# Kernel tuning notes

Measured on AMD Instinct MI355X. Metric: run time of the kernel, lower is better.

## Reference

```python
import jax, jax.numpy as jnp
import numpy as np

B, T, H = 16, 512, 768
S = 32            # gold spans per example
L = 50            # max_span_len -> candidate ends per span
NT = 3            # num_types
HS = 4 * H        # span repr size


def setup_inputs() -> dict:
    key = jax.random.key(0)
    ks = jax.random.split(key, 8)
    h = jax.random.normal(ks[0], (B, T, H), dtype=jnp.float32)
    attention_mask = jnp.ones((B, T), dtype=jnp.int32)
    starts = jax.random.randint(ks[1], (B, S), 1, 400).astype(jnp.int32)
    lens = jax.random.randint(ks[2], (B, S), 0, L).astype(jnp.int32)
    ends = starts + lens                      # <= 448 < last_tok=510
    types = jax.random.randint(ks[3], (B, S), 0, NT).astype(jnp.int32)
    W1 = jax.random.normal(ks[4], (HS, HS), dtype=jnp.float32) * (1.0 / np.sqrt(HS))
    b1 = jnp.zeros((HS,), dtype=jnp.float32)
    w_score = jax.random.normal(ks[5], (HS,), dtype=jnp.float32) * (1.0 / np.sqrt(HS))
    b_score = jnp.zeros((1,), dtype=jnp.float32)
    W_type = jax.random.normal(ks[6], (HS, NT), dtype=jnp.float32) * (1.0 / np.sqrt(HS))
    b_type = jnp.zeros((NT,), dtype=jnp.float32)
    return {"h": h, "attention_mask": attention_mask, "span_starts": starts,
            "span_ends": ends, "span_types": types, "W1": W1, "b1": b1,
            "w_score": w_score, "b_score": b_score, "W_type": W_type, "b_type": b_type}


def _span_loss(h, attention_mask, span_starts, span_ends, span_types,
               W1, b1, w_score, b_score, W_type, b_type, type_loss_weight=1.0):
    cls = h[:, 0]                                              # [B,H]
    # prefix sums for O(1) segment means: pre[b,t] = sum h[b,0:t]
    pre = jnp.concatenate([jnp.zeros((B, 1, H), h.dtype), jnp.cumsum(h, axis=1)], axis=1)

    valid_len = attention_mask.sum(axis=1)                     # [B]
    last_tok = jnp.maximum(1, valid_len - 2)                   # [B]

    s = span_starts                                            # [B,S]
    e_gold = span_ends
    gold_idx = e_gold - s                                      # [B,S]
    lt = last_tok[:, None]
    span_valid = (s >= 1) & (s <= lt) & (e_gold >= s) & (e_gold <= lt) & (gold_idx < L)

    e_max = jnp.minimum(s + L - 1, lt)                         # [B,S]
    p = s[..., None] + jnp.arange(L, dtype=s.dtype)            # [B,S,L] candidate ends
    cand_valid = p <= e_max[..., None]

    sc = jnp.clip(s, 0, T - 1)
    pc = jnp.clip(p, 0, T - 1)
    bi2 = jnp.arange(B)[:, None]
    bi3 = jnp.arange(B)[:, None, None]

    h_start = h[bi2, sc]                                       # [B,S,H]
    h_end = h[bi3, pc]                                         # [B,S,L,H]
    seg_len = jnp.maximum(p - s[..., None] + 1, 1).astype(h.dtype)
    h_mean = (pre[bi3, pc + 1] - pre[bi2, sc][:, :, None]) / seg_len[..., None]

    repr_ = jnp.concatenate([
        jnp.broadcast_to(h_start[:, :, None], (B, S, L, H)),
        h_end,
        h_mean,
        jnp.broadcast_to(cls[:, None, None], (B, S, L, H)),
    ], axis=-1)                                                # [B,S,L,4H]

    h1 = jax.nn.gelu(jnp.einsum('bslh,hd->bsld', repr_, W1) + b1, approximate=False)
    scores = jnp.einsum('bsld,d->bsl', h1, w_score) + b_score[0]      # [B,S,L]
    type_logits = jnp.einsum('bsld,dk->bslk', h1, W_type) + b_type    # [B,S,L,NT]

    # end-index CE over valid candidate ends
    masked = jnp.where(cand_valid, scores, jnp.float32(-1e9))
    logp_end = jax.nn.log_softmax(masked, axis=-1)             # [B,S,L]
    gi = jnp.clip(gold_idx, 0, L - 1)
    end_loss = -jnp.take_along_axis(logp_end, gi[..., None], axis=-1)[..., 0]  # [B,S]

    # type CE at the gold end index
    tl_gold = jnp.take_along_axis(type_logits, gi[..., None, None], axis=2)[:, :, 0]  # [B,S,NT]
    logp_t = jax.nn.log_softmax(tl_gold, axis=-1)
    tg = jnp.clip(span_types, 0, NT - 1)
    type_loss = -jnp.take_along_axis(logp_t, tg[..., None], axis=-1)[..., 0]  # [B,S]

    vmask = span_valid.astype(h.dtype)
    n_seg = vmask.sum()
    denom = jnp.maximum(n_seg, 1.0)
    loss_end = jnp.where(n_seg > 0, (end_loss * vmask).sum() / denom, 0.0)
    loss_type = jnp.where(n_seg > 0, (type_loss * vmask).sum() / denom, 0.0)
    return loss_end + type_loss_weight * loss_type


def reference(h, attention_mask, span_starts, span_ends, span_types,
              W1, b1, w_score, b_score, W_type, b_type):
    return _span_loss(h, attention_mask, span_starts, span_ends, span_types,
                      W1, b1, w_score, b_score, W_type, b_type)
```

## Files before the change

kernel.cpp:

```cpp
#include <hip/hip_runtime.h>
#include <hip/hip_bf16.h>
#include <math.h>

#define B_ 16
#define T_ 512
#define H_ 768
#define S_ 32
#define L_ 50
#define NT_ 3
#define HS_ 3072
#define CH_ 32
#define CT_ 16

#define TX_ 464
#define YB2 7424
#define GB 14848
#define CLSB 15360
#define XYROWS 14848
#define AROWS 15616
#define NKT 24
#define SLOT_SH 16384

typedef __attribute__((ext_vector_type(8))) short short8;
typedef __attribute__((ext_vector_type(4))) float f32x4;

__device__ __forceinline__ unsigned short f2bf(float f) {
    __hip_bfloat16 b = __float2bfloat16(f);
    return *(unsigned short*)&b;
}
__device__ __forceinline__ float bf2f(unsigned short u) {
    union { unsigned int i; float f; } v; v.i = ((unsigned int)u) << 16; return v.f;
}
__device__ __forceinline__ void load_lds16(const void* g, void* l) {
    __builtin_amdgcn_global_load_lds((__attribute__((address_space(1))) void*)g,
                                     (__attribute__((address_space(3))) void*)l, 16, 0, 0);
}
__device__ __forceinline__ ushort4 pack4(float4 v) {
    ushort4 o; o.x = f2bf(v.x); o.y = f2bf(v.y); o.z = f2bf(v.z); o.w = f2bf(v.w);
    return o;
}

__device__ __forceinline__ float gelu_exact(float v) {
    float a = fabsf(v) * 0.70710678118654752f;
    float t = __builtin_amdgcn_rcpf(fmaf(a, 0.47047f, 1.0f));
    float poly = t * fmaf(t, fmaf(t, 0.7478556f, -0.0958798f), 0.3480242f);
    float e = __builtin_amdgcn_exp2f(a * a * -1.4426950408889634f);
    float erfa = fmaf(-poly, e, 1.0f);
    float erfv = copysignf(erfa, v);
    return 0.5f * v * (1.0f + erfv);
}

__global__ __launch_bounds__(256) void cumsum_pass1(const float4* __restrict__ h4,
                                                    float4* __restrict__ partial) {
    int idx = blockIdx.x * 256 + threadIdx.x;
    int hd4 = idx % 192; int t = idx / 192; int ch = t % CH_; int b = t / CH_;
    const float4* hp = h4 + ((size_t)b * T_ + ch * CT_) * 192 + hd4;
    float4 acc = {0.f, 0.f, 0.f, 0.f};
#pragma unroll
    for (int tt = 0; tt < CT_; tt++) {
        float4 v = hp[(size_t)tt * 192];
        acc.x += v.x; acc.y += v.y; acc.z += v.z; acc.w += v.w;
    }
    partial[idx] = acc;
}

__global__ __launch_bounds__(256) void cumsum_pass3(const float4* __restrict__ h4,
                                                    const float4* __restrict__ partial,
                                                    ushort4* __restrict__ Ab4) {
    int idx = blockIdx.x * 256 + threadIdx.x;
    int hd4 = idx % 192; int t = idx / 192; int ch = t % CH_; int b = t / CH_;
    if (ch * CT_ >= TX_) return;
    float4 acc = {0.f, 0.f, 0.f, 0.f};
#pragma unroll
    for (int c = 0; c < CH_; c++) {
        if (c < ch) {
            float4 v = partial[((size_t)b * CH_ + c) * 192 + hd4];
            acc.x += v.x; acc.y += v.y; acc.z += v.z; acc.w += v.w;
        }
    }
    const float4* hp = h4 + ((size_t)b * T_ + ch * CT_) * 192 + hd4;
    if (ch == 0) {
        ushort4 z = {0, 0, 0, 0};
        Ab4[((size_t)(YB2 + b * TX_)) * 192 + hd4] = z;
    }
#pragma unroll
    for (int tt = 0; tt < CT_; tt++) {
        int t2 = ch * CT_ + tt;
        float4 hv = hp[(size_t)tt * 192];
        if (t2 < TX_)
            Ab4[((size_t)(b * TX_ + t2)) * 192 + hd4] = pack4(hv);
        acc.x += hv.x; acc.y += hv.y; acc.z += hv.z; acc.w += hv.w;
        if (t2 + 1 < TX_)
            Ab4[((size_t)(YB2 + b * TX_ + t2 + 1)) * 192 + hd4] = pack4(acc);
    }
}

__global__ void gather_kernel(const float* __restrict__ h,
                              const int* __restrict__ starts,
                              __hip_bfloat16* __restrict__ Ab) {
    int r = blockIdx.x;
    int src_row, dst_row;
    if (r < B_ * S_) {
        int b = r / S_;
        int sv = starts[r];
        int sc = min(max(sv, 0), T_ - 1);
        src_row = b * T_ + sc;
        dst_row = GB + r;
    } else {
        int b = r - B_ * S_;
        src_row = b * T_;
        dst_row = CLSB + b;
    }
    __hip_bfloat16* dst = Ab + (size_t)dst_row * H_;
    const float* src = h + (size_t)src_row * H_;
    for (int j = threadIdx.x; j < H_; j += 256)
        dst[j] = __float2bfloat16(src[j]);
}

__global__ __launch_bounds__(256) void transpose_w(const float* __restrict__ W1,
                                                   __hip_bfloat16* __restrict__ Wt) {
    __shared__ float tile[64][65];
    int n0 = blockIdx.x * 64, k0 = blockIdx.y * 64;
    int c = threadIdx.x & 63, r0 = threadIdx.x >> 6;
#pragma unroll
    for (int i = 0; i < 16; i++) {
        int r = r0 + i * 4;
        tile[r][c] = W1[(size_t)(k0 + r) * HS_ + n0 + c];
    }
    __syncthreads();
    int p = k0 / H_, kl = k0 % H_;
    __hip_bfloat16* out = Wt + (size_t)p * HS_ * H_;
#pragma unroll
    for (int i = 0; i < 16; i++) {
        int r = r0 + i * 4;
        out[(size_t)(n0 + r) * H_ + kl + c] = __float2bfloat16(tile[c][r]);
    }
}

__device__ __forceinline__ void mfma16(const short8 (&a)[4], const short8 (&b)[4],
                                       f32x4 (&acc)[8][4], int off) {
#pragma unroll
    for (int mf = 0; mf < 4; ++mf)
#pragma unroll
        for (int nf = 0; nf < 4; ++nf)
            acc[off + mf][nf] = __builtin_amdgcn_mfma_f32_16x16x32_bf16(
                a[mf], b[nf], acc[off + mf][nf], 0, 0, 0);
}

#define STAGE_A(nslot, k0_) {                                                  \
    char* d_ = (char*)(nslot) + dstoff;                                        \
    load_lds16(pA + (k0_), d_);                                                \
    load_lds16(pA + (size_t)128 * H_ + (k0_), d_ + 8192);                      \
}
#define STAGE_B(nslot, k0_) {                                                  \
    char* d_ = (char*)(nslot) + 16384 + dstoff;                                \
    load_lds16(pB + (k0_), d_);                                                \
    load_lds16(pB + (size_t)128 * H_ + (k0_), d_ + 8192);                      \
}

#define TILE_STEP(kt, WAITSTR, DO_STAGE)                                       \
  {                                                                            \
    const short* slot = lds + ((kt) & 3) * SLOT_SH;                            \
    short* nslot = lds + (((kt) + 3) & 3) * SLOT_SH;                           \
    asm volatile(WAITSTR ::: "memory");                                        \
    __builtin_amdgcn_s_barrier();                                              \
    __builtin_amdgcn_sched_barrier(0);                                         \
    short8 a[4], b[4];                                                         \
    _Pragma("unroll")                                                          \
    for (int i = 0; i < 4; ++i)                                                \
      a[i] = *(const short8*)&slot[(wr * 128 + i * 16 + l15) * 32 + pcs];      \
    _Pragma("unroll")                                                          \
    for (int i = 0; i < 4; ++i)                                                \
      b[i] = *(const short8*)&slot[8192 + (wc * 64 + i * 16 + l15) * 32 + pcs];\
    if (DO_STAGE) { STAGE_A(nslot, ((kt) + 3) * 32) }                          \
    asm volatile("s_waitcnt lgkmcnt(0)" ::: "memory");                         \
    __builtin_amdgcn_sched_barrier(0);                                         \
    __builtin_amdgcn_s_setprio(1);                                             \
    mfma16(a, b, acc, 0);                                                      \
    __builtin_amdgcn_s_setprio(0);                                             \
    __builtin_amdgcn_s_barrier();                                              \
    __builtin_amdgcn_sched_barrier(0);                                         \
    _Pragma("unroll")                                                          \
    for (int i = 0; i < 4; ++i)                                                \
      a[i] = *(const short8*)&slot[(wr * 128 + 64 + i * 16 + l15) * 32 + pcs]; \
    if (DO_STAGE) { STAGE_B(nslot, ((kt) + 3) * 32) }                          \
    asm volatile("s_waitcnt lgkmcnt(0)" ::: "memory");                         \
    __builtin_amdgcn_sched_barrier(0);                                         \
    __builtin_amdgcn_s_setprio(1);                                             \
    mfma16(a, b, acc, 4);                                                      \
    __builtin_amdgcn_s_setprio(0);                                             \
  }

__global__ __launch_bounds__(512, 2) void mfma_gemm(const __hip_bfloat16* __restrict__ Ab,
                                                    const __hip_bfloat16* __restrict__ Wt,
                                                    __hip_bfloat16* __restrict__ XY,
                                                    float* __restrict__ ST,
                                                    float* __restrict__ CC) {
    __shared__ short lds[4 * SLOT_SH];
    int tid = threadIdx.x;
    int wave = tid >> 6, lane = tid & 63;
    int wr = wave >> 2, wc = wave & 3;
    int l15 = lane & 15;
    int pcs = ((lane >> 4) ^ ((l15 >> 1) & 3)) * 8;

    int orig = blockIdx.x;
    int xcd = orig & 7, loc = orig >> 3;
    int wg = (xcd < 4 ? xcd * 92 : 368 + (xcd - 4) * 91) + loc;
    int mt = wg / 12, nt = wg - mt * 12;
    int m0 = mt << 8, n0 = nt << 8;

    const __hip_bfloat16* Bt;
    if (m0 < YB2)        Bt = Wt + (size_t)1 * HS_ * H_;
    else if (m0 < GB)    Bt = Wt + (size_t)2 * HS_ * H_;
    else if (m0 < CLSB)  Bt = Wt;
    else                 Bt = Wt + (size_t)3 * HS_ * H_;

    int srow = wave * 16 + (lane >> 2);
    int lcS = ((lane & 3) ^ ((lane >> 3) & 3)) * 8;
    const __hip_bfloat16* pA = Ab + (size_t)(m0 + srow) * H_ + lcS;
    const __hip_bfloat16* pB = Bt + (size_t)(n0 + srow) * H_ + lcS;
    int dstoff = wave * 1024;

    f32x4 acc[8][4] = {};

#pragma unroll
    for (int t = 0; t < 3; ++t) {
        STAGE_A(lds + t * SLOT_SH, t * 32)
        STAGE_B(lds + t * SLOT_SH, t * 32)
    }

    for (int kt = 0; kt < NKT - 3; ++kt)
        TILE_STEP(kt, "s_waitcnt vmcnt(8)", true)
    TILE_STEP(NKT - 3, "s_waitcnt vmcnt(8)", false)
    TILE_STEP(NKT - 2, "s_waitcnt vmcnt(4)", false)
    TILE_STEP(NKT - 1, "s_waitcnt vmcnt(0)", false)

    int mb = m0 + wr * 128, nb = n0 + wc * 64;
#pragma unroll
    for (int mf = 0; mf < 8; ++mf) {
#pragma unroll
        for (int nf = 0; nf < 4; ++nf) {
            int n = nb + nf * 16 + l15;
            int mr = mb + mf * 16 + (lane >> 4) * 4;
#pragma unroll
            for (int r = 0; r < 4; ++r) {
                int m = mr + r;
                float v = acc[mf][nf][r];
                if (m < XYROWS) {
                    XY[(size_t)m * HS_ + n] = __float2bfloat16(v);
                } else if (m < CLSB) {
                    ST[(size_t)(m - GB) * HS_ + n] = v;
                } else if (m < CLSB + 16) {
                    CC[(size_t)(m - CLSB) * HS_ + n] = v;
                }
            }
        }
    }
}

__global__ __launch_bounds__(256) void c0_kernel(const float4* __restrict__ ST,
                                                 const float4* __restrict__ CC,
                                                 const float4* __restrict__ b1,
                                                 const float4* __restrict__ w_score,
                                                 ushort4* __restrict__ c0b,
                                                 ushort4* __restrict__ wb16) {
    if (blockIdx.x >= 512 * HS_ / 4 / 256) {
        int i = (blockIdx.x - 512 * HS_ / 4 / 256) * 256 + threadIdx.x;
        wb16[i] = pack4(w_score[i]);
        return;
    }
    int i = blockIdx.x * 256 + threadIdx.x;
    int row = i / (HS_ / 4);
    int b = row >> 5;
    int c4 = i % (HS_ / 4);
    float4 s = ST[i], c = CC[b * (HS_ / 4) + c4], bb = b1[c4];
    float4 v = {s.x + c.x + bb.x, s.y + c.y + bb.y, s.z + c.z + bb.z, s.w + c.w + bb.w};
    c0b[i] = pack4(v);
}

__global__ __launch_bounds__(256) void combine_kernel(
    const unsigned short* __restrict__ c0, const unsigned short* __restrict__ wb16,
    const __hip_bfloat16* __restrict__ XY,
    const float* __restrict__ b_score, const float* __restrict__ W_type,
    const int* __restrict__ starts, const int* __restrict__ ends,
    float* __restrict__ scores, float* __restrict__ tgold) {
    int x = blockIdx.x;
    int b = x & 15, s = x >> 4;
    int bs = b * S_ + s;
    int wave = threadIdx.x >> 6, lane = threadIdx.x & 63;
    int pr = blockIdx.y * 4 + wave;
    if (pr >= L_ / 2) return;
    int l0 = pr * 2, l1 = l0 + 1;
    int sv = starts[bs], ev = ends[bs];
    int gi = min(max(ev - sv, 0), L_ - 1);
    int sc = min(max(sv, 0), TX_ - 1);
    int pc0 = min(max(sv + l0, 0), TX_ - 2);
    int pc1 = min(max(sv + l1, 0), TX_ - 2);
    float inv0 = 1.0f / (float)(l0 + 1);
    float inv1 = 1.0f / (float)(l1 + 1);
    bool isg0 = (l0 == gi), isg1 = (l1 == gi);
    bool anyg = isg0 || isg1;

    const unsigned short* X0 = (const unsigned short*)(XY + (size_t)(b * TX_ + pc0) * HS_);
    const unsigned short* X1 = (const unsigned short*)(XY + (size_t)(b * TX_ + pc1) * HS_);
    const unsigned short* Y0 = (const unsigned short*)(XY + (size_t)(YB2 + b * TX_ + pc0 + 1) * HS_);
    const unsigned short* Y1 = (const unsigned short*)(XY + (size_t)(YB2 + b * TX_ + pc1 + 1) * HS_);
    const unsigned short* Ysr = (const unsigned short*)(XY + (size_t)(YB2 + b * TX_ + sc) * HS_);
    const unsigned short* c0r = c0 + (size_t)bs * HS_;

    float local0 = 0.f, local1 = 0.f, t0 = 0.f, t1 = 0.f, t2 = 0.f;
#pragma unroll
    for (int j = 0; j < 6; j++) {
        int d = j * 512 + lane * 8;
        short8 xv0 = *(const short8*)(X0 + d);
        short8 xv1 = *(const short8*)(X1 + d);
        short8 yv0 = *(const short8*)(Y0 + d);
        short8 yv1 = *(const short8*)(Y1 + d);
        short8 sv8 = *(const short8*)(Ysr + d);
        short8 cv8 = *(const short8*)(c0r + d);
        short8 wv8 = *(const short8*)(wb16 + d);
#pragma unroll
        for (int q = 0; q < 8; q++) {
            float ys = bf2f(((const unsigned short*)&sv8)[q]);
            float cv = bf2f(((const unsigned short*)&cv8)[q]);
            float w  = bf2f(((const unsigned short*)&wv8)[q]);
            float v0 = fmaf(bf2f(((const unsigned short*)&yv0)[q]) - ys, inv0, cv) +
                       bf2f(((const unsigned short*)&xv0)[q]);
            float v1 = fmaf(bf2f(((const unsigned short*)&yv1)[q]) - ys, inv1, cv) +
                       bf2f(((const unsigned short*)&xv1)[q]);
            float g0 = gelu_exact(v0);
            float g1 = gelu_exact(v1);
            local0 = fmaf(g0, w, local0);
            local1 = fmaf(g1, w, local1);
            if (anyg) {
                float gg = isg0 ? g0 : g1;
                t0 = fmaf(gg, W_type[(d + q) * NT_ + 0], t0);
                t1 = fmaf(gg, W_type[(d + q) * NT_ + 1], t1);
                t2 = fmaf(gg, W_type[(d + q) * NT_ + 2], t2);
            }
        }
    }
#pragma unroll
    for (int off = 32; off >= 1; off >>= 1) {
        local0 += __shfl_down(local0, off);
        local1 += __shfl_down(local1, off);
    }
    if (lane == 0) {
        float bs0 = b_score[0];
        scores[(size_t)bs * L_ + l0] = local0 + bs0;
        scores[(size_t)bs * L_ + l1] = local1 + bs0;
    }
    if (anyg) {
#pragma unroll
        for (int off = 32; off >= 1; off >>= 1) {
            t0 += __shfl_down(t0, off);
            t1 += __shfl_down(t1, off);
            t2 += __shfl_down(t2, off);
        }
        if (lane == 0) {
            tgold[bs * NT_ + 0] = t0;
            tgold[bs * NT_ + 1] = t1;
            tgold[bs * NT_ + 2] = t2;
        }
    }
}

__global__ __launch_bounds__(512) void loss_kernel(
    const float* __restrict__ scores, const float* __restrict__ tgold,
    const int* __restrict__ mask, const int* __restrict__ starts,
    const int* __restrict__ ends, const int* __restrict__ types,
    const float* __restrict__ b_type, float* __restrict__ out) {
    __shared__ int svl[B_];
    __shared__ float r[3][8];
    int tid = threadIdx.x;
    int b = tid / S_;
    if (tid < B_) svl[tid] = 0;
    __syncthreads();
    {
        int part = 0;
        const int* mp = mask + tid * 16;
#pragma unroll
        for (int i = 0; i < 16; i++) part += mp[i];
        atomicAdd(&svl[tid / (T_ / 16)], part);
    }
    __syncthreads();
    int vl = svl[b];
    int lt = max(1, vl - 2);
    int sv = starts[tid], ev = ends[tid];
    int gold = ev - sv;
    bool valid = (sv >= 1) && (sv <= lt) && (ev >= sv) && (ev <= lt) && (gold < L_);
    int emax = min(sv + L_ - 1, lt);
    const float* sp = scores + (size_t)tid * L_;
    float m = -1e30f;
    for (int l = 0; l < L_; l++) {
        float v = (sv + l <= emax) ? sp[l] : -1e9f;
        m = fmaxf(m, v);
    }
    float sum = 0.f;
    for (int l = 0; l < L_; l++) {
        float v = (sv + l <= emax) ? sp[l] : -1e9f;
        sum += expf(v - m);
    }
    int gi = min(max(gold, 0), L_ - 1);
    float vg = (sv + gi <= emax) ? sp[gi] : -1e9f;
    float end_loss = (m + logf(sum)) - vg;

    float t0 = tgold[tid * 3 + 0] + b_type[0];
    float t1 = tgold[tid * 3 + 1] + b_type[1];
    float t2 = tgold[tid * 3 + 2] + b_type[2];
    float tm = fmaxf(t0, fmaxf(t1, t2));
    float tsum = expf(t0 - tm) + expf(t1 - tm) + expf(t2 - tm);
    int tg = min(max(types[tid], 0), NT_ - 1);
    float tv = (tg == 0) ? t0 : ((tg == 1) ? t1 : t2);
    float type_loss = (tm + logf(tsum)) - tv;

    float ve = valid ? end_loss : 0.f;
    float vt = valid ? type_loss : 0.f;
    float vc = valid ? 1.f : 0.f;
    for (int off = 32; off >= 1; off >>= 1) {
        ve += __shfl_down(ve, off);
        vt += __shfl_down(vt, off);
        vc += __shfl_down(vc, off);
    }
    if ((tid & 63) == 0) {
        int w = tid >> 6;
        r[0][w] = ve; r[1][w] = vt; r[2][w] = vc;
    }
    __syncthreads();
    if (tid == 0) {
        float se = 0, st = 0, n = 0;
        for (int w = 0; w < 8; w++) { se += r[0][w]; st += r[1][w]; n += r[2][w]; }
        float denom = fmaxf(n, 1.f);
        out[0] = (n > 0.f) ? (se / denom + st / denom) : 0.f;
    }
}

extern "C" void kernel_launch(void* const* d_in, const int* in_sizes, int n_in,
                              void* d_out, int out_size, void* d_ws, size_t ws_size,
                              hipStream_t stream) {
    const float* h       = (const float*)d_in[0];
    const int*   mask    = (const int*)d_in[1];
    const int*   starts  = (const int*)d_in[2];
    const int*   ends    = (const int*)d_in[3];
    const int*   types   = (const int*)d_in[4];
    const float* W1      = (const float*)d_in[5];
    const float* b1      = (const float*)d_in[6];
    const float* w_score = (const float*)d_in[7];
    const float* b_score = (const float*)d_in[8];
    const float* W_type  = (const float*)d_in[9];
    const float* b_type  = (const float*)d_in[10];
    float* out = (float*)d_out;

    char* ws = (char*)d_ws;
    size_t off = 0;
    __hip_bfloat16* Ab = (__hip_bfloat16*)(ws + off); off += (size_t)AROWS * H_ * 2;
    __hip_bfloat16* XY = (__hip_bfloat16*)(ws + off); off += (size_t)XYROWS * HS_ * 2;
    __hip_bfloat16* Wt = (__hip_bfloat16*)(ws + off); off += (size_t)4 * HS_ * H_ * 2;
    float* ST     = (float*)(ws + off);               off += (size_t)512 * HS_ * 4;
    float* CC     = (float*)(ws + off);               off += (size_t)16 * HS_ * 4;
    unsigned short* c0b = (unsigned short*)(ws + off); off += (size_t)512 * HS_ * 2;
    unsigned short* wb16 = (unsigned short*)(ws + off); off += (size_t)HS_ * 2;
    float* scores = (float*)(ws + off);               off += (size_t)B_ * S_ * L_ * 4;
    float* tgold  = (float*)(ws + off);               off += (size_t)B_ * S_ * NT_ * 4;
    float4* partial = (float4*)XY;

    hipLaunchKernelGGL(cumsum_pass1, dim3(B_ * CH_ * 192 / 256), dim3(256), 0, stream,
                       (const float4*)h, partial);
    hipLaunchKernelGGL(cumsum_pass3, dim3(B_ * CH_ * 192 / 256), dim3(256), 0, stream,
                       (const float4*)h, (const float4*)partial, (ushort4*)Ab);
    hipLaunchKernelGGL(gather_kernel, dim3(B_ * S_ + B_), dim3(256), 0, stream, h, starts, Ab);
    hipLaunchKernelGGL(transpose_w, dim3(48, 48), dim3(256), 0, stream, W1, Wt);
    hipLaunchKernelGGL(mfma_gemm, dim3((AROWS / 256) * 12), dim3(512), 0, stream,
                       Ab, Wt, XY, ST, CC);
    hipLaunchKernelGGL(c0_kernel, dim3(512 * HS_ / 4 / 256 + 3), dim3(256), 0, stream,
                       (const float4*)ST, (const float4*)CC, (const float4*)b1,
                       (const float4*)w_score, (ushort4*)c0b, (ushort4*)wb16);
    hipLaunchKernelGGL(combine_kernel, dim3(B_ * S_, 7), dim3(256), 0, stream,
                       c0b, wb16, XY, b_score, W_type, starts, ends, scores, tgold);
    hipLaunchKernelGGL(loss_kernel, dim3(1), dim3(512), 0, stream,
                       scores, tgold, mask, starts, ends, types, b_type, out);
}
```

Baseline: 317.2 us.

## Fuse gather into cumsum pass and c0 into combine, drop GEMM sched barrier

Merges the gather kernel into cumsum_pass3 as extra blocks, and removes the c0_kernel by computing ST+CC+b1 and the bf16 w_score inside combine_kernel, whose grid shrinks from 7 y-blocks to 1 with each wave looping over span-length pairs. It also drops one sched_barrier in the GEMM inner loop. The aim is fewer launches and no c0b/wb16 round trip through memory. In exchange, combine has less parallelism (512 blocks instead of about 3584), holds the per-span c0 vector in registers, and the GEMM instruction schedule may shift.

```diff
diff --git a/kernel.cpp b/kernel.cpp
--- a/kernel.cpp
+++ b/kernel.cpp
@@ -66,7 +66,29 @@
 
 __global__ __launch_bounds__(256) void cumsum_pass3(const float4* __restrict__ h4,
                                                     const float4* __restrict__ partial,
-                                                    ushort4* __restrict__ Ab4) {
+                                                    ushort4* __restrict__ Ab4,
+                                                    const float* __restrict__ h,
+                                                    const int* __restrict__ starts) {
+    if (blockIdx.x >= B_ * CH_ * 192 / 256) {
+        int r = blockIdx.x - B_ * CH_ * 192 / 256;
+        int src_row, dst_row;
+        if (r < B_ * S_) {
+            int b = r / S_;
+            int sv = starts[r];
+            int sc = min(max(sv, 0), T_ - 1);
+            src_row = b * T_ + sc;
+            dst_row = GB + r;
+        } else {
+            int b = r - B_ * S_;
+            src_row = b * T_;
+            dst_row = CLSB + b;
+        }
+        __hip_bfloat16* dst = (__hip_bfloat16*)Ab4 + (size_t)dst_row * H_;
+        const float* src = h + (size_t)src_row * H_;
+        for (int j = threadIdx.x; j < H_; j += 256)
+            dst[j] = __float2bfloat16(src[j]);
+        return;
+    }
     int idx = blockIdx.x * 256 + threadIdx.x;
     int hd4 = idx % 192; int t = idx / 192; int ch = t % CH_; int b = t / CH_;
     if (ch * CT_ >= TX_) return;
@@ -93,28 +115,6 @@
         if (t2 + 1 < TX_)
             Ab4[((size_t)(YB2 + b * TX_ + t2 + 1)) * 192 + hd4] = pack4(acc);
     }
-}
-
-__global__ void gather_kernel(const float* __restrict__ h,
-                              const int* __restrict__ starts,
-                              __hip_bfloat16* __restrict__ Ab) {
-    int r = blockIdx.x;
-    int src_row, dst_row;
-    if (r < B_ * S_) {
-        int b = r / S_;
-        int sv = starts[r];
-        int sc = min(max(sv, 0), T_ - 1);
-        src_row = b * T_ + sc;
-        dst_row = GB + r;
-    } else {
-        int b = r - B_ * S_;
-        src_row = b * T_;
-        dst_row = CLSB + b;
-    }
-    __hip_bfloat16* dst = Ab + (size_t)dst_row * H_;
-    const float* src = h + (size_t)src_row * H_;
-    for (int j = threadIdx.x; j < H_; j += 256)
-        dst[j] = __float2bfloat16(src[j]);
 }
 
 __global__ __launch_bounds__(256) void transpose_w(const float* __restrict__ W1,
@@ -179,7 +179,6 @@
     mfma16(a, b, acc, 0);                                                      \
     __builtin_amdgcn_s_setprio(0);                                             \
     __builtin_amdgcn_s_barrier();                                              \
-    __builtin_amdgcn_sched_barrier(0);                                         \
     _Pragma("unroll")                                                          \
     for (int i = 0; i < 4; ++i)                                                \
       a[i] = *(const short8*)&slot[(wr * 128 + 64 + i * 16 + l15) * 32 + pcs]; \
@@ -258,28 +257,9 @@
     }
 }
 
-__global__ __launch_bounds__(256) void c0_kernel(const float4* __restrict__ ST,
-                                                 const float4* __restrict__ CC,
-                                                 const float4* __restrict__ b1,
-                                                 const float4* __restrict__ w_score,
-                                                 ushort4* __restrict__ c0b,
-                                                 ushort4* __restrict__ wb16) {
-    if (blockIdx.x >= 512 * HS_ / 4 / 256) {
-        int i = (blockIdx.x - 512 * HS_ / 4 / 256) * 256 + threadIdx.x;
-        wb16[i] = pack4(w_score[i]);
-        return;
-    }
-    int i = blockIdx.x * 256 + threadIdx.x;
-    int row = i / (HS_ / 4);
-    int b = row >> 5;
-    int c4 = i % (HS_ / 4);
-    float4 s = ST[i], c = CC[b * (HS_ / 4) + c4], bb = b1[c4];
-    float4 v = {s.x + c.x + bb.x, s.y + c.y + bb.y, s.z + c.z + bb.z, s.w + c.w + bb.w};
-    c0b[i] = pack4(v);
-}
-
 __global__ __launch_bounds__(256) void combine_kernel(
-    const unsigned short* __restrict__ c0, const unsigned short* __restrict__ wb16,
+    const float* __restrict__ ST, const float* __restrict__ CC,
+    const float* __restrict__ b1, const float* __restrict__ w_score,
     const __hip_bfloat16* __restrict__ XY,
     const float* __restrict__ b_score, const float* __restrict__ W_type,
     const int* __restrict__ starts, const int* __restrict__ ends,
@@ -288,79 +268,100 @@
     int b = x & 15, s = x >> 4;
     int bs = b * S_ + s;
     int wave = threadIdx.x >> 6, lane = threadIdx.x & 63;
-    int pr = blockIdx.y * 4 + wave;
-    if (pr >= L_ / 2) return;
-    int l0 = pr * 2, l1 = l0 + 1;
     int sv = starts[bs], ev = ends[bs];
     int gi = min(max(ev - sv, 0), L_ - 1);
     int sc = min(max(sv, 0), TX_ - 1);
-    int pc0 = min(max(sv + l0, 0), TX_ - 2);
-    int pc1 = min(max(sv + l1, 0), TX_ - 2);
-    float inv0 = 1.0f / (float)(l0 + 1);
-    float inv1 = 1.0f / (float)(l1 + 1);
-    bool isg0 = (l0 == gi), isg1 = (l1 == gi);
-    bool anyg = isg0 || isg1;
-
-    const unsigned short* X0 = (const unsigned short*)(XY + (size_t)(b * TX_ + pc0) * HS_);
-    const unsigned short* X1 = (const unsigned short*)(XY + (size_t)(b * TX_ + pc1) * HS_);
-    const unsigned short* Y0 = (const unsigned short*)(XY + (size_t)(YB2 + b * TX_ + pc0 + 1) * HS_);
-    const unsigned short* Y1 = (const unsigned short*)(XY + (size_t)(YB2 + b * TX_ + pc1 + 1) * HS_);
+    float bs0 = b_score[0];
+
+    union U8 { short8 s; unsigned short u[8]; };
+    short8 ysv[6], cv[6], wv[6];
     const unsigned short* Ysr = (const unsigned short*)(XY + (size_t)(YB2 + b * TX_ + sc) * HS_);
-    const unsigned short* c0r = c0 + (size_t)bs * HS_;
-
-    float local0 = 0.f, local1 = 0.f, t0 = 0.f, t1 = 0.f, t2 = 0.f;
+    const float* STr = ST + (size_t)bs * HS_;
+    const float* CCr = CC + (size_t)b * HS_;
 #pragma unroll
     for (int j = 0; j < 6; j++) {
         int d = j * 512 + lane * 8;
-        short8 xv0 = *(const short8*)(X0 + d);
-        short8 xv1 = *(const short8*)(X1 + d);
-        short8 yv0 = *(const short8*)(Y0 + d);
-        short8 yv1 = *(const short8*)(Y1 + d);
-        short8 sv8 = *(const short8*)(Ysr + d);
-        short8 cv8 = *(const short8*)(c0r + d);
-        short8 wv8 = *(const short8*)(wb16 + d);
-#pragma unroll
-        for (int q = 0; q < 8; q++) {
-            float ys = bf2f(((const unsigned short*)&sv8)[q]);
-            float cv = bf2f(((const unsigned short*)&cv8)[q]);
-            float w  = bf2f(((const unsigned short*)&wv8)[q]);
-            float v0 = fmaf(bf2f(((const unsigned short*)&yv0)[q]) - ys, inv0, cv) +
-                       bf2f(((const unsigned short*)&xv0)[q]);
-            float v1 = fmaf(bf2f(((const unsigned short*)&yv1)[q]) - ys, inv1, cv) +
-                       bf2f(((const unsigned short*)&xv1)[q]);
-            float g0 = gelu_exact(v0);
-            float g1 = gelu_exact(v1);
-            local0 = fmaf(g0, w, local0);
-            local1 = fmaf(g1, w, local1);
-            if (anyg) {
-                float gg = isg0 ? g0 : g1;
-                t0 = fmaf(gg, W_type[(d + q) * NT_ + 0], t0);
-                t1 = fmaf(gg, W_type[(d + q) * NT_ + 1], t1);
-                t2 = fmaf(gg, W_type[(d + q) * NT_ + 2], t2);
+        ysv[j] = *(const short8*)(Ysr + d);
+        float4 sa = *(const float4*)(STr + d),     sb = *(const float4*)(STr + d + 4);
+        float4 ca = *(const float4*)(CCr + d),     cb = *(const float4*)(CCr + d + 4);
+        float4 ba = *(const float4*)(b1 + d),      bb = *(const float4*)(b1 + d + 4);
+        U8 uc;
+        uc.u[0] = f2bf(sa.x + ca.x + ba.x); uc.u[1] = f2bf(sa.y + ca.y + ba.y);
+        uc.u[2] = f2bf(sa.z + ca.z + ba.z); uc.u[3] = f2bf(sa.w + ca.w + ba.w);
+        uc.u[4] = f2bf(sb.x + cb.x + bb.x); uc.u[5] = f2bf(sb.y + cb.y + bb.y);
+        uc.u[6] = f2bf(sb.z + cb.z + bb.z); uc.u[7] = f2bf(sb.w + cb.w + bb.w);
+        cv[j] = uc.s;
+        float4 wa = *(const float4*)(w_score + d), wb = *(const float4*)(w_score + d + 4);
+        U8 uw;
+        uw.u[0] = f2bf(wa.x); uw.u[1] = f2bf(wa.y); uw.u[2] = f2bf(wa.z); uw.u[3] = f2bf(wa.w);
+        uw.u[4] = f2bf(wb.x); uw.u[5] = f2bf(wb.y); uw.u[6] = f2bf(wb.z); uw.u[7] = f2bf(wb.w);
+        wv[j] = uw.s;
+    }
+
+    for (int pr = wave; pr < L_ / 2; pr += 4) {
+        int l0 = pr * 2, l1 = l0 + 1;
+        int pc0 = min(max(sv + l0, 0), TX_ - 2);
+        int pc1 = min(max(sv + l1, 0), TX_ - 2);
+        float inv0 = 1.0f / (float)(l0 + 1);
+        float inv1 = 1.0f / (float)(l1 + 1);
+        bool isg0 = (l0 == gi), isg1 = (l1 == gi);
+        bool anyg = isg0 || isg1;
+
+        const unsigned short* X0 = (const unsigned short*)(XY + (size_t)(b * TX_ + pc0) * HS_);
+        const unsigned short* X1 = (const unsigned short*)(XY + (size_t)(b * TX_ + pc1) * HS_);
+        const unsigned short* Y0 = (const unsigned short*)(XY + (size_t)(YB2 + b * TX_ + pc0 + 1) * HS_);
+        const unsigned short* Y1 = (const unsigned short*)(XY + (size_t)(YB2 + b * TX_ + pc1 + 1) * HS_);
+
+        float local0 = 0.f, local1 = 0.f, t0 = 0.f, t1 = 0.f, t2 = 0.f;
+#pragma unroll
+        for (int j = 0; j < 6; j++) {
+            int d = j * 512 + lane * 8;
+            short8 xv0 = *(const short8*)(X0 + d);
+            short8 xv1 = *(const short8*)(X1 + d);
+            short8 yv0 = *(const short8*)(Y0 + d);
+            short8 yv1 = *(const short8*)(Y1 + d);
+#pragma unroll
+            for (int q = 0; q < 8; q++) {
+                float ys = bf2f(((const unsigned short*)&ysv[j])[q]);
+                float cvq = bf2f(((const unsigned short*)&cv[j])[q]);
+                float w  = bf2f(((const unsigned short*)&wv[j])[q]);
+                float v0 = fmaf(bf2f(((const unsigned short*)&yv0)[q]) - ys, inv0, cvq) +
+                           bf2f(((const unsigned short*)&xv0)[q]);
+                float v1 = fmaf(bf2f(((const unsigned short*)&yv1)[q]) - ys, inv1, cvq) +
+                           bf2f(((const unsigned short*)&xv1)[q]);
+                float g0 = gelu_exact(v0);
+                float g1 = gelu_exact(v1);
+                local0 = fmaf(g0, w, local0);
+                local1 = fmaf(g1, w, local1);
+                if (anyg) {
+                    float gg = isg0 ? g0 : g1;
+                    t0 = fmaf(gg, W_type[(d + q) * NT_ + 0], t0);
+                    t1 = fmaf(gg, W_type[(d + q) * NT_ + 1], t1);
+                    t2 = fmaf(gg, W_type[(d + q) * NT_ + 2], t2);
+                }
             }
         }
-    }
-#pragma unroll
-    for (int off = 32; off >= 1; off >>= 1) {
-        local0 += __shfl_down(local0, off);
-        local1 += __shfl_down(local1, off);
-    }
-    if (lane == 0) {
-        float bs0 = b_score[0];
-        scores[(size_t)bs * L_ + l0] = local0 + bs0;
-        scores[(size_t)bs * L_ + l1] = local1 + bs0;
-    }
-    if (anyg) {
 #pragma unroll
         for (int off = 32; off >= 1; off >>= 1) {
-            t0 += __shfl_down(t0, off);
-            t1 += __shfl_down(t1, off);
-            t2 += __shfl_down(t2, off);
+            local0 += __shfl_down(local0, off);
+            local1 += __shfl_down(local1, off);
         }
         if (lane == 0) {
-            tgold[bs * NT_ + 0] = t0;
-            tgold[bs * NT_ + 1] = t1;
-            tgold[bs * NT_ + 2] = t2;
+            scores[(size_t)bs * L_ + l0] = local0 + bs0;
+            scores[(size_t)bs * L_ + l1] = local1 + bs0;
+        }
+        if (anyg) {
+#pragma unroll
+            for (int off = 32; off >= 1; off >>= 1) {
+                t0 += __shfl_down(t0, off);
+                t1 += __shfl_down(t1, off);
+                t2 += __shfl_down(t2, off);
+            }
+            if (lane == 0) {
+                tgold[bs * NT_ + 0] = t0;
+                tgold[bs * NT_ + 1] = t1;
+                tgold[bs * NT_ + 2] = t2;
+            }
         }
     }
 }
@@ -458,25 +459,21 @@
     __hip_bfloat16* Wt = (__hip_bfloat16*)(ws + off); off += (size_t)4 * HS_ * H_ * 2;
     float* ST     = (float*)(ws + off);               off += (size_t)512 * HS_ * 4;
     float* CC     = (float*)(ws + off);               off += (size_t)16 * HS_ * 4;
-    unsigned short* c0b = (unsigned short*)(ws + off); off += (size_t)512 * HS_ * 2;
-    unsigned short* wb16 = (unsigned short*)(ws + off); off += (size_t)HS_ * 2;
     float* scores = (float*)(ws + off);               off += (size_t)B_ * S_ * L_ * 4;
     float* tgold  = (float*)(ws + off);               off += (size_t)B_ * S_ * NT_ * 4;
     float4* partial = (float4*)XY;
 
     hipLaunchKernelGGL(cumsum_pass1, dim3(B_ * CH_ * 192 / 256), dim3(256), 0, stream,
                        (const float4*)h, partial);
-    hipLaunchKernelGGL(cumsum_pass3, dim3(B_ * CH_ * 192 / 256), dim3(256), 0, stream,
-                       (const float4*)h, (const float4*)partial, (ushort4*)Ab);
-    hipLaunchKernelGGL(gather_kernel, dim3(B_ * S_ + B_), dim3(256), 0, stream, h, starts, Ab);
+    hipLaunchKernelGGL(cumsum_pass3, dim3(B_ * CH_ * 192 / 256 + B_ * S_ + B_), dim3(256),
+                       0, stream, (const float4*)h, (const float4*)partial, (ushort4*)Ab,
+                       h, starts);
     hipLaunchKernelGGL(transpose_w, dim3(48, 48), dim3(256), 0, stream, W1, Wt);
     hipLaunchKernelGGL(mfma_gemm, dim3((AROWS / 256) * 12), dim3(512), 0, stream,
                        Ab, Wt, XY, ST, CC);
-    hipLaunchKernelGGL(c0_kernel, dim3(512 * HS_ / 4 / 256 + 3), dim3(256), 0, stream,
-                       (const float4*)ST, (const float4*)CC, (const float4*)b1,
-                       (const float4*)w_score, (ushort4*)c0b, (ushort4*)wb16);
-    hipLaunchKernelGGL(combine_kernel, dim3(B_ * S_, 7), dim3(256), 0, stream,
-                       c0b, wb16, XY, b_score, W_type, starts, ends, scores, tgold);
+    hipLaunchKernelGGL(combine_kernel, dim3(B_ * S_), dim3(256), 0, stream,
+                       ST, CC, b1, w_score, XY, b_score, W_type, starts, ends,
+                       scores, tgold);
     hipLaunchKernelGGL(loss_kernel, dim3(1), dim3(512), 0, stream,
                        scores, tgold, mask, starts, ends, types, b_type, out);
 }
```

Measured after the change: 371.8 us. +17.2%, slower.

## Restructure combine kernel around token windows staged in LDS; fuse gather into cumsum

Applied to the files above, without the earlier changes.

The combine kernel is reorganized so each block owns a window of 5 token positions for one batch row. It stages the X/Y rows for those positions and the score weights into LDS, then iterates over all spans whose candidate ends fall in the window. Each X/Y row is read from global memory once per window rather than once per (span, candidate) pair, which cuts redundant HBM/L2 traffic. The gather kernel is folded into cumsum_pass3 as extra blocks, saving a launch, and one sched_barrier is dropped in the GEMM macro. The trade-offs are a serial loop over all 32 spans per block, uneven work per window, and higher LDS use (about 66KB) that limits occupancy.

```diff
diff --git a/kernel.cpp b/kernel.cpp
--- a/kernel.cpp
+++ b/kernel.cpp
@@ -20,6 +20,8 @@
 #define AROWS 15616
 #define NKT 24
 #define SLOT_SH 16384
+#define WW 5
+#define NWIN 90
 
 typedef __attribute__((ext_vector_type(8))) short short8;
 typedef __attribute__((ext_vector_type(4))) float f32x4;
@@ -66,7 +68,29 @@
 
 __global__ __launch_bounds__(256) void cumsum_pass3(const float4* __restrict__ h4,
                                                     const float4* __restrict__ partial,
-                                                    ushort4* __restrict__ Ab4) {
+                                                    ushort4* __restrict__ Ab4,
+                                                    const float* __restrict__ h,
+                                                    const int* __restrict__ starts) {
+    if (blockIdx.x >= B_ * CH_ * 192 / 256) {
+        int r = blockIdx.x - B_ * CH_ * 192 / 256;
+        int src_row, dst_row;
+        if (r < B_ * S_) {
+            int b = r / S_;
+            int sv = starts[r];
+            int sc = min(max(sv, 0), T_ - 1);
+            src_row = b * T_ + sc;
+            dst_row = GB + r;
+        } else {
+            int b = r - B_ * S_;
+            src_row = b * T_;
+            dst_row = CLSB + b;
+        }
+        __hip_bfloat16* dst = (__hip_bfloat16*)Ab4 + (size_t)dst_row * H_;
+        const float* src = h + (size_t)src_row * H_;
+        for (int j = threadIdx.x; j < H_; j += 256)
+            dst[j] = __float2bfloat16(src[j]);
+        return;
+    }
     int idx = blockIdx.x * 256 + threadIdx.x;
     int hd4 = idx % 192; int t = idx / 192; int ch = t % CH_; int b = t / CH_;
     if (ch * CT_ >= TX_) return;
@@ -93,28 +117,6 @@
         if (t2 + 1 < TX_)
             Ab4[((size_t)(YB2 + b * TX_ + t2 + 1)) * 192 + hd4] = pack4(acc);
     }
-}
-
-__global__ void gather_kernel(const float* __restrict__ h,
-                              const int* __restrict__ starts,
-                              __hip_bfloat16* __restrict__ Ab) {
-    int r = blockIdx.x;
-    int src_row, dst_row;
-    if (r < B_ * S_) {
-        int b = r / S_;
-        int sv = starts[r];
-        int sc = min(max(sv, 0), T_ - 1);
-        src_row = b * T_ + sc;
-        dst_row = GB + r;
-    } else {
-        int b = r - B_ * S_;
-        src_row = b * T_;
-        dst_row = CLSB + b;
-    }
-    __hip_bfloat16* dst = Ab + (size_t)dst_row * H_;
-    const float* src = h + (size_t)src_row * H_;
-    for (int j = threadIdx.x; j < H_; j += 256)
-        dst[j] = __float2bfloat16(src[j]);
 }
 
 __global__ __launch_bounds__(256) void transpose_w(const float* __restrict__ W1,
@@ -179,7 +181,6 @@
     mfma16(a, b, acc, 0);                                                      \
     __builtin_amdgcn_s_setprio(0);                                             \
     __builtin_amdgcn_s_barrier();                                              \
-    __builtin_amdgcn_sched_barrier(0);                                         \
     _Pragma("unroll")                                                          \
     for (int i = 0; i < 4; ++i)                                                \
       a[i] = *(const short8*)&slot[(wr * 128 + 64 + i * 16 + l15) * 32 + pcs]; \
@@ -278,90 +279,101 @@
     c0b[i] = pack4(v);
 }
 
-__global__ __launch_bounds__(256) void combine_kernel(
-    const unsigned short* __restrict__ c0, const unsigned short* __restrict__ wb16,
+__global__ __launch_bounds__(512, 4) void combine_kernel(
+    const unsigned short* __restrict__ c0b, const unsigned short* __restrict__ wb16,
     const __hip_bfloat16* __restrict__ XY,
     const float* __restrict__ b_score, const float* __restrict__ W_type,
     const int* __restrict__ starts, const int* __restrict__ ends,
     float* __restrict__ scores, float* __restrict__ tgold) {
+    __shared__ unsigned short xL[WW * HS_];
+    __shared__ unsigned short yL[WW * HS_];
+    __shared__ unsigned short wL[HS_];
     int x = blockIdx.x;
-    int b = x & 15, s = x >> 4;
-    int bs = b * S_ + s;
-    int wave = threadIdx.x >> 6, lane = threadIdx.x & 63;
-    int pr = blockIdx.y * 4 + wave;
-    if (pr >= L_ / 2) return;
-    int l0 = pr * 2, l1 = l0 + 1;
-    int sv = starts[bs], ev = ends[bs];
-    int gi = min(max(ev - sv, 0), L_ - 1);
-    int sc = min(max(sv, 0), TX_ - 1);
-    int pc0 = min(max(sv + l0, 0), TX_ - 2);
-    int pc1 = min(max(sv + l1, 0), TX_ - 2);
-    float inv0 = 1.0f / (float)(l0 + 1);
-    float inv1 = 1.0f / (float)(l1 + 1);
-    bool isg0 = (l0 == gi), isg1 = (l1 == gi);
-    bool anyg = isg0 || isg1;
-
-    const unsigned short* X0 = (const unsigned short*)(XY + (size_t)(b * TX_ + pc0) * HS_);
-    const unsigned short* X1 = (const unsigned short*)(XY + (size_t)(b * TX_ + pc1) * HS_);
-    const unsigned short* Y0 = (const unsigned short*)(XY + (size_t)(YB2 + b * TX_ + pc0 + 1) * HS_);
-    const unsigned short* Y1 = (const unsigned short*)(XY + (size_t)(YB2 + b * TX_ + pc1 + 1) * HS_);
-    const unsigned short* Ysr = (const unsigned short*)(XY + (size_t)(YB2 + b * TX_ + sc) * HS_);
-    const unsigned short* c0r = c0 + (size_t)bs * HS_;
-
-    float local0 = 0.f, local1 = 0.f, t0 = 0.f, t1 = 0.f, t2 = 0.f;
-#pragma unroll
-    for (int j = 0; j < 6; j++) {
-        int d = j * 512 + lane * 8;
-        short8 xv0 = *(const short8*)(X0 + d);
-        short8 xv1 = *(const short8*)(X1 + d);
-        short8 yv0 = *(const short8*)(Y0 + d);
-        short8 yv1 = *(const short8*)(Y1 + d);
-        short8 sv8 = *(const short8*)(Ysr + d);
-        short8 cv8 = *(const short8*)(c0r + d);
-        short8 wv8 = *(const short8*)(wb16 + d);
-#pragma unroll
-        for (int q = 0; q < 8; q++) {
-            float ys = bf2f(((const unsigned short*)&sv8)[q]);
-            float cv = bf2f(((const unsigned short*)&cv8)[q]);
-            float w  = bf2f(((const unsigned short*)&wv8)[q]);
-            float v0 = fmaf(bf2f(((const unsigned short*)&yv0)[q]) - ys, inv0, cv) +
-                       bf2f(((const unsigned short*)&xv0)[q]);
-            float v1 = fmaf(bf2f(((const unsigned short*)&yv1)[q]) - ys, inv1, cv) +
-                       bf2f(((const unsigned short*)&xv1)[q]);
-            float g0 = gelu_exact(v0);
-            float g1 = gelu_exact(v1);
-            local0 = fmaf(g0, w, local0);
-            local1 = fmaf(g1, w, local1);
-            if (anyg) {
-                float gg = isg0 ? g0 : g1;
-                t0 = fmaf(gg, W_type[(d + q) * NT_ + 0], t0);
-                t1 = fmaf(gg, W_type[(d + q) * NT_ + 1], t1);
-                t2 = fmaf(gg, W_type[(d + q) * NT_ + 2], t2);
+    int b = x & 15, wnd = x >> 4;
+    int t0 = wnd * WW;
+    int tid = threadIdx.x;
+    int wave = tid >> 6, lane = tid & 63;
+
+    const unsigned short* Xbase = (const unsigned short*)XY + (size_t)(b * TX_) * HS_;
+    const unsigned short* Ybase = (const unsigned short*)XY + (size_t)(YB2 + b * TX_ + 1) * HS_;
+    for (int idx = tid * 8; idx < WW * HS_; idx += 512 * 8) {
+        load_lds16(Xbase + (size_t)t0 * HS_ + idx, (char*)xL + (size_t)idx * 2);
+        load_lds16(Ybase + (size_t)t0 * HS_ + idx, (char*)yL + (size_t)idx * 2);
+    }
+    if (tid * 8 < HS_)
+        load_lds16(wb16 + tid * 8, (char*)wL + (size_t)tid * 16);
+    __syncthreads();
+
+    float bs0 = b_score[0];
+    int tcount = 0;
+    for (int s = 0; s < S_; s++) {
+        int bs = b * S_ + s;
+        int sv = starts[bs];
+        int lmin = max(0, t0 - sv);
+        int lmax = min(L_ - 1, t0 + WW - 1 - sv);
+        if (lmax < lmin) continue;
+        int c = lmax - lmin + 1;
+        int off = ((wave - tcount) % 8 + 8) % 8;
+        for (int i = off; i < c; i += 8) {
+            int l = lmin + i;
+            int pcc = sv + l;
+            int ri = pcc - t0;
+            float inv = 1.0f / (float)(l + 1);
+            int ev = ends[bs];
+            int gi = min(max(ev - sv, 0), L_ - 1);
+            bool isg = (l == gi);
+            int sc = min(max(sv, 0), TX_ - 1);
+            const unsigned short* Xr = &xL[ri * HS_];
+            const unsigned short* Yr = &yL[ri * HS_];
+            const unsigned short* Ysr = (const unsigned short*)XY +
+                                        (size_t)(YB2 + b * TX_ + sc) * HS_;
+            const unsigned short* c0r = c0b + (size_t)bs * HS_;
+
+            float local = 0.f, t0a = 0.f, t1a = 0.f, t2a = 0.f;
+#pragma unroll 2
+            for (int j = 0; j < 6; j++) {
+                int d = j * 512 + lane * 8;
+                short8 xv = *(const short8*)&Xr[d];
+                short8 yv = *(const short8*)&Yr[d];
+                short8 ys8 = *(const short8*)(Ysr + d);
+                short8 cv8 = *(const short8*)(c0r + d);
+                short8 wv8 = *(const short8*)&wL[d];
+#pragma unroll
+                for (int q = 0; q < 8; q++) {
+                    float ys = bf2f(((const unsigned short*)&ys8)[q]);
+                    float cvq = bf2f(((const unsigned short*)&cv8)[q]);
+                    float w = bf2f(((const unsigned short*)&wv8)[q]);
+                    float v = fmaf(bf2f(((const unsigned short*)&yv)[q]) - ys, inv, cvq) +
+                              bf2f(((const unsigned short*)&xv)[q]);
+                    float g = gelu_exact(v);
+                    local = fmaf(g, w, local);
+                    if (isg) {
+                        t0a = fmaf(g, W_type[(d + q) * NT_ + 0], t0a);
+                        t1a = fmaf(g, W_type[(d + q) * NT_ + 1], t1a);
+                        t2a = fmaf(g, W_type[(d + q) * NT_ + 2], t2a);
+                    }
+                }
+            }
+#pragma unroll
+            for (int o = 32; o >= 1; o >>= 1)
+                local += __shfl_down(local, o);
+            if (lane == 0)
+                scores[(size_t)bs * L_ + l] = local + bs0;
+            if (isg) {
+#pragma unroll
+                for (int o = 32; o >= 1; o >>= 1) {
+                    t0a += __shfl_down(t0a, o);
+                    t1a += __shfl_down(t1a, o);
+                    t2a += __shfl_down(t2a, o);
+                }
+                if (lane == 0) {
+                    tgold[bs * NT_ + 0] = t0a;
+                    tgold[bs * NT_ + 1] = t1a;
+                    tgold[bs * NT_ + 2] = t2a;
+                }
             }
         }
-    }
-#pragma unroll
-    for (int off = 32; off >= 1; off >>= 1) {
-        local0 += __shfl_down(local0, off);
-        local1 += __shfl_down(local1, off);
-    }
-    if (lane == 0) {
-        float bs0 = b_score[0];
-        scores[(size_t)bs * L_ + l0] = local0 + bs0;
-        scores[(size_t)bs * L_ + l1] = local1 + bs0;
-    }
-    if (anyg) {
-#pragma unroll
-        for (int off = 32; off >= 1; off >>= 1) {
-            t0 += __shfl_down(t0, off);
-            t1 += __shfl_down(t1, off);
-            t2 += __shfl_down(t2, off);
-        }
-        if (lane == 0) {
-            tgold[bs * NT_ + 0] = t0;
-            tgold[bs * NT_ + 1] = t1;
-            tgold[bs * NT_ + 2] = t2;
-        }
+        tcount += c;
     }
 }
 
@@ -466,16 +478,16 @@
 
     hipLaunchKernelGGL(cumsum_pass1, dim3(B_ * CH_ * 192 / 256), dim3(256), 0, stream,
                        (const float4*)h, partial);
-    hipLaunchKernelGGL(cumsum_pass3, dim3(B_ * CH_ * 192 / 256), dim3(256), 0, stream,
-                       (const float4*)h, (const float4*)partial, (ushort4*)Ab);
-    hipLaunchKernelGGL(gather_kernel, dim3(B_ * S_ + B_), dim3(256), 0, stream, h, starts, Ab);
+    hipLaunchKernelGGL(cumsum_pass3, dim3(B_ * CH_ * 192 / 256 + B_ * S_ + B_), dim3(256),
+                       0, stream, (const float4*)h, (const float4*)partial, (ushort4*)Ab,
+                       h, starts);
     hipLaunchKernelGGL(transpose_w, dim3(48, 48), dim3(256), 0, stream, W1, Wt);
     hipLaunchKernelGGL(mfma_gemm, dim3((AROWS / 256) * 12), dim3(512), 0, stream,
                        Ab, Wt, XY, ST, CC);
     hipLaunchKernelGGL(c0_kernel, dim3(512 * HS_ / 4 / 256 + 3), dim3(256), 0, stream,
                        (const float4*)ST, (const float4*)CC, (const float4*)b1,
                        (const float4*)w_score, (ushort4*)c0b, (ushort4*)wb16);
-    hipLaunchKernelGGL(combine_kernel, dim3(B_ * S_, 7), dim3(256), 0, stream,
+    hipLaunchKernelGGL(combine_kernel, dim3(NWIN * 16), dim3(512), 0, stream,
                        c0b, wb16, XY, b_score, W_type, starts, ends, scores, tgold);
     hipLaunchKernelGGL(loss_kernel, dim3(1), dim3(512), 0, stream,
                        scores, tgold, mask, starts, ends, types, b_type, out);
```

After: 335.1 us. +5.6%, slower.
